# Kernel tuning notes

Measured on AMD Instinct MI355X. Metric: run time of the kernel, lower is better.

The kernel has to match this reference:

```python
import jax, jax.numpy as jnp
import numpy as np

N_FILTERS = 8
FILTER_LEN = 31
PAD = (FILTER_LEN - 1) // 2  # 15
B, L = 64, 131072


def setup_inputs() -> dict:
    key = jax.random.key(0)
    ks = jax.random.split(key, 7)
    x = jax.random.normal(ks[0], (B, L), dtype=jnp.float32)
    features = jax.random.normal(ks[1], (B, N_FILTERS), dtype=jnp.float32)
    # learned params
    filter_params = jax.random.normal(ks[2], (N_FILTERS, 1, FILTER_LEN), dtype=jnp.float32)
    # selector MLP (torch Linear convention: W is (out, in))
    lim = 1.0 / np.sqrt(N_FILTERS)
    W1 = jax.random.uniform(ks[3], (N_FILTERS, N_FILTERS), minval=-lim, maxval=lim, dtype=jnp.float32)
    b1 = jax.random.uniform(ks[4], (N_FILTERS,), minval=-lim, maxval=lim, dtype=jnp.float32)
    W2 = jax.random.uniform(ks[5], (N_FILTERS, N_FILTERS), minval=-lim, maxval=lim, dtype=jnp.float32)
    b2 = jax.random.uniform(ks[6], (N_FILTERS,), minval=-lim, maxval=lim, dtype=jnp.float32)
    return {"x": x, "features": features, "filter_params": filter_params,
            "W1": W1, "b1": b1, "W2": W2, "b2": b2}


def reference(x, features, filter_params, W1, b1, W2, b2):
    # conv1d (cross-correlation, as in torch): (B,1,L) * (F,1,K) -> (B,F,L)
    xp = x[:, None, :]
    filtered = jax.lax.conv_general_dilated(
        xp, filter_params,
        window_strides=(1,), padding=[(PAD, PAD)],
        dimension_numbers=('NCH', 'OIH', 'NCH'))
    # per-sample soft filter selection
    h = jax.nn.relu(features @ W1.T + b1)
    weights = jax.nn.softmax(h @ W2.T + b2, axis=-1)  # (B, F)
    # weighted sum over filter channels -> (B, L)
    out = jnp.einsum('bfl,bf->bl', filtered, weights)
    return out
```

## Files before the change

### kernel.cpp

```cpp
#include <hip/hip_runtime.h>
#include <math.h>

#define BB 64
#define LL 131072
#define NF 8
#define FLEN 31

#define TPB 256
#define NWAVE 4
#define RPT 8
#define TILE (TPB * RPT)
#define TCELLS (TILE / 4)
#define WCELLS 128
#define WSTAGE (WCELLS + 8)
#define ROWCELLS (LL / 4)

typedef float f32x4 __attribute__((ext_vector_type(4)));

#define SWZ(c) ((c) ^ (((c) >> 3) & 7))

__global__ __launch_bounds__(TPB, 6) void adaptive_filter_fused(
    const float* __restrict__ x,
    const float* __restrict__ features,
    const float* __restrict__ fp,
    const float* __restrict__ W1,
    const float* __restrict__ b1,
    const float* __restrict__ W2,
    const float* __restrict__ b2,
    float* __restrict__ out)
{
    const int tiles_per_row = LL / TILE;
    const int row  = blockIdx.x / tiles_per_row;
    const int tile = blockIdx.x % tiles_per_row;
    const int tid  = threadIdx.x;
    const int wv   = tid >> 6;
    const int ln   = tid & 63;

    __shared__ f32x4 lds4[NWAVE][WSTAGE];
    __shared__ float cs[NWAVE][32];

    const f32x4* xrow4 = reinterpret_cast<const f32x4*>(x + (size_t)row * LL);
    const int wcell0 = tile * TCELLS + wv * WCELLS;
    const int cell_base = wcell0 - 4;

    const int d0 = ln, d1 = ln + 64;
    const unsigned gc0 = (unsigned)(cell_base + d0);
    const unsigned gc1 = (unsigned)(cell_base + d1);
    f32x4 v0 = (f32x4)(0.0f);
    f32x4 v1 = v0, v2 = v0;
    if (gc0 < ROWCELLS) v0 = __builtin_nontemporal_load(&xrow4[gc0]);
    if (gc1 < ROWCELLS) v1 = __builtin_nontemporal_load(&xrow4[gc1]);
    const bool has2 = (ln < WSTAGE - 128);
    const unsigned gc2 = (unsigned)(cell_base + ln + 128);
    if (has2 && gc2 < ROWCELLS) v2 = __builtin_nontemporal_load(&xrow4[gc2]);

    if (ln < FLEN) {
        const int t = ln;
        float f[NF];
        #pragma unroll
        for (int j = 0; j < NF; ++j) f[j] = features[row * NF + j];

        float h[NF];
        #pragma unroll
        for (int i = 0; i < NF; ++i) {
            float s = b1[i];
            #pragma unroll
            for (int j = 0; j < NF; ++j) s = fmaf(f[j], W1[i * NF + j], s);
            h[i] = fmaxf(s, 0.0f);
        }

        float w[NF];
        float m = -1e30f;
        #pragma unroll
        for (int i = 0; i < NF; ++i) {
            float s = b2[i];
            #pragma unroll
            for (int j = 0; j < NF; ++j) s = fmaf(h[j], W2[i * NF + j], s);
            w[i] = s;
            m = fmaxf(m, s);
        }
        float denom = 0.0f;
        #pragma unroll
        for (int i = 0; i < NF; ++i) { w[i] = expf(w[i] - m); denom += w[i]; }
        const float inv = 1.0f / denom;

        float s = 0.0f;
        #pragma unroll
        for (int ff = 0; ff < NF; ++ff) s = fmaf(w[ff] * inv, fp[ff * FLEN + t], s);
        cs[wv][t] = s;
    }

    lds4[wv][SWZ(d0)] = v0;
    lds4[wv][SWZ(d1)] = v1;
    if (has2) lds4[wv][SWZ(ln + 128)] = v2;


    const float tv = cs[wv][ln & 31];
    float tap[FLEN];
    #pragma unroll
    for (int t = 0; t < FLEN; ++t)
        tap[t] = __int_as_float(__builtin_amdgcn_readlane(__float_as_int(tv), t));

    float wA[20], wB[20];
    #pragma unroll
    for (int k = 0; k < 5; ++k) {
        const f32x4 v = lds4[wv][SWZ(2 * ln + k)];
        wA[4 * k + 0] = v.x; wA[4 * k + 1] = v.y;
        wA[4 * k + 2] = v.z; wA[4 * k + 3] = v.w;
    }
    #pragma unroll
    for (int k = 0; k < 5; ++k) {
        const f32x4 v = lds4[wv][SWZ(2 * ln + 5 + k)];
        wB[4 * k + 0] = v.x; wB[4 * k + 1] = v.y;
        wB[4 * k + 2] = v.z; wB[4 * k + 3] = v.w;
    }

    float acc[RPT];
    #pragma unroll
    for (int r = 0; r < RPT; ++r) acc[r] = 0.0f;

    #pragma unroll
    for (int r = 0; r < RPT; ++r) {
        #pragma unroll
        for (int t = 0; t <= 18 - r; ++t)
            acc[r] = fmaf(tap[t], wA[r + 1 + t], acc[r]);
        #pragma unroll
        for (int t = 19 - r; t < FLEN; ++t)
            acc[r] = fmaf(tap[t], wB[r + t - 19], acc[r]);
    }

    f32x4* orow4 = reinterpret_cast<f32x4*>(out + (size_t)row * LL) + wcell0;
    f32x4 s0; s0.x = acc[0]; s0.y = acc[1]; s0.z = acc[2]; s0.w = acc[3];
    f32x4 s1; s1.x = acc[4]; s1.y = acc[5]; s1.z = acc[6]; s1.w = acc[7];
    __builtin_nontemporal_store(s0, &orow4[2 * ln + 0]);
    __builtin_nontemporal_store(s1, &orow4[2 * ln + 1]);
}

extern "C" void kernel_launch(void* const* d_in, const int* in_sizes, int n_in,
                              void* d_out, int out_size, void* d_ws, size_t ws_size,
                              hipStream_t stream) {
    const float* x        = (const float*)d_in[0];
    const float* features = (const float*)d_in[1];
    const float* fp       = (const float*)d_in[2];
    const float* W1       = (const float*)d_in[3];
    const float* b1       = (const float*)d_in[4];
    const float* W2       = (const float*)d_in[5];
    const float* b2       = (const float*)d_in[6];
    float* out = (float*)d_out;

    const int grid = BB * (LL / TILE);
    adaptive_filter_fused<<<grid, TPB, 0, stream>>>(x, features, fp, W1, b1, W2, b2, out);
}
```

Before: 22.02 us.

## Use single-wave blocks and keep combined taps in registers instead of LDS

Blocks shrink from four waves to one, so each block handles one wave-sized tile and the grid grows fourfold. Every lane now computes the MLP/softmax and combined tap, using a clamped index, and the taps are broadcast with readlane directly, without going through the LDS scratch array. The launch-bounds occupancy hint is dropped. The change relies on single-wave lockstep for LDS ordering and adds more, smaller blocks with extra launch and scheduling overhead. Lanes past the 31 taps now do redundant MLP work.

```diff
diff --git a/kernel.cpp b/kernel.cpp
--- a/kernel.cpp
+++ b/kernel.cpp
@@ -6,20 +6,18 @@
 #define NF 8
 #define FLEN 31
 
-#define TPB 256
-#define NWAVE 4
+#define TPB 64
 #define RPT 8
 #define TILE (TPB * RPT)
 #define TCELLS (TILE / 4)
-#define WCELLS 128
-#define WSTAGE (WCELLS + 8)
+#define NCELLS (TCELLS + 8)
 #define ROWCELLS (LL / 4)
 
 typedef float f32x4 __attribute__((ext_vector_type(4)));
 
 #define SWZ(c) ((c) ^ (((c) >> 3) & 7))
 
-__global__ __launch_bounds__(TPB, 6) void adaptive_filter_fused(
+__global__ __launch_bounds__(TPB) void adaptive_filter_fused(
     const float* __restrict__ x,
     const float* __restrict__ features,
     const float* __restrict__ fp,
@@ -32,30 +30,28 @@
     const int tiles_per_row = LL / TILE;
     const int row  = blockIdx.x / tiles_per_row;
     const int tile = blockIdx.x % tiles_per_row;
-    const int tid  = threadIdx.x;
-    const int wv   = tid >> 6;
-    const int ln   = tid & 63;
+    const int ln   = threadIdx.x;
 
-    __shared__ f32x4 lds4[NWAVE][WSTAGE];
-    __shared__ float cs[NWAVE][32];
+    __shared__ f32x4 lds4[NCELLS];
 
     const f32x4* xrow4 = reinterpret_cast<const f32x4*>(x + (size_t)row * LL);
-    const int wcell0 = tile * TCELLS + wv * WCELLS;
+    const int wcell0 = tile * TCELLS;
     const int cell_base = wcell0 - 4;
 
     const int d0 = ln, d1 = ln + 64;
     const unsigned gc0 = (unsigned)(cell_base + d0);
     const unsigned gc1 = (unsigned)(cell_base + d1);
+    const unsigned gc2 = (unsigned)(cell_base + ln + 128);
     f32x4 v0 = (f32x4)(0.0f);
     f32x4 v1 = v0, v2 = v0;
     if (gc0 < ROWCELLS) v0 = __builtin_nontemporal_load(&xrow4[gc0]);
     if (gc1 < ROWCELLS) v1 = __builtin_nontemporal_load(&xrow4[gc1]);
-    const bool has2 = (ln < WSTAGE - 128);
-    const unsigned gc2 = (unsigned)(cell_base + ln + 128);
+    const bool has2 = (ln < NCELLS - 128);
     if (has2 && gc2 < ROWCELLS) v2 = __builtin_nontemporal_load(&xrow4[gc2]);
 
-    if (ln < FLEN) {
-        const int t = ln;
+    const int t = ln < FLEN ? ln : (FLEN - 1);
+    float taps_mine;
+    {
         float f[NF];
         #pragma unroll
         for (int j = 0; j < NF; ++j) f[j] = features[row * NF + j];
@@ -87,30 +83,28 @@
         float s = 0.0f;
         #pragma unroll
         for (int ff = 0; ff < NF; ++ff) s = fmaf(w[ff] * inv, fp[ff * FLEN + t], s);
-        cs[wv][t] = s;
+        taps_mine = s;
     }
 
-    lds4[wv][SWZ(d0)] = v0;
-    lds4[wv][SWZ(d1)] = v1;
-    if (has2) lds4[wv][SWZ(ln + 128)] = v2;
-
-
-    const float tv = cs[wv][ln & 31];
     float tap[FLEN];
     #pragma unroll
-    for (int t = 0; t < FLEN; ++t)
-        tap[t] = __int_as_float(__builtin_amdgcn_readlane(__float_as_int(tv), t));
+    for (int k = 0; k < FLEN; ++k)
+        tap[k] = __int_as_float(__builtin_amdgcn_readlane(__float_as_int(taps_mine), k));
+
+    lds4[SWZ(d0)] = v0;
+    lds4[SWZ(d1)] = v1;
+    if (has2) lds4[SWZ(ln + 128)] = v2;
 
     float wA[20], wB[20];
     #pragma unroll
     for (int k = 0; k < 5; ++k) {
-        const f32x4 v = lds4[wv][SWZ(2 * ln + k)];
+        const f32x4 v = lds4[SWZ(2 * ln + k)];
         wA[4 * k + 0] = v.x; wA[4 * k + 1] = v.y;
         wA[4 * k + 2] = v.z; wA[4 * k + 3] = v.w;
     }
     #pragma unroll
     for (int k = 0; k < 5; ++k) {
-        const f32x4 v = lds4[wv][SWZ(2 * ln + 5 + k)];
+        const f32x4 v = lds4[SWZ(2 * ln + 5 + k)];
         wB[4 * k + 0] = v.x; wB[4 * k + 1] = v.y;
         wB[4 * k + 2] = v.z; wB[4 * k + 3] = v.w;
     }
@@ -122,11 +116,11 @@
     #pragma unroll
     for (int r = 0; r < RPT; ++r) {
         #pragma unroll
-        for (int t = 0; t <= 18 - r; ++t)
-            acc[r] = fmaf(tap[t], wA[r + 1 + t], acc[r]);
+        for (int k = 0; k <= 18 - r; ++k)
+            acc[r] = fmaf(tap[k], wA[r + 1 + k], acc[r]);
         #pragma unroll
-        for (int t = 19 - r; t < FLEN; ++t)
-            acc[r] = fmaf(tap[t], wB[r + t - 19], acc[r]);
+        for (int k = 19 - r; k < FLEN; ++k)
+            acc[r] = fmaf(tap[k], wB[r + k - 19], acc[r]);
     }
 
     f32x4* orow4 = reinterpret_cast<f32x4*>(out + (size_t)row * LL) + wcell0;
```

Result: no change. 22.27 us (+1.1%).
